# Optimization experiments

Hardware: AMD Instinct MI355X
Metric: run time of the kernel (lower is better)

The kernel has to match this reference:

```python
import jax, jax.numpy as jnp
import numpy as np

B, S, HID, NH = 4, 2048, 512, 8
DH = HID // NH
NEG = -1000000.0


def setup_inputs() -> dict:
    key = jax.random.key(0)
    ks = jax.random.split(key, 8)
    scale = 1.0 / np.sqrt(HID)
    return {
        "queries": jax.random.normal(ks[0], (B, S, HID), dtype=jnp.float32),
        "keys": jax.random.normal(ks[1], (B, S, HID), dtype=jnp.float32),
        "values": jax.random.normal(ks[2], (B, S, HID), dtype=jnp.float32),
        "valid_lens": jax.random.randint(ks[3], (B,), 1, S + 1, dtype=jnp.int32),
        "Wq": jax.random.uniform(ks[4], (HID, HID), jnp.float32, -scale, scale),
        "Wk": jax.random.uniform(ks[5], (HID, HID), jnp.float32, -scale, scale),
        "Wv": jax.random.uniform(ks[6], (HID, HID), jnp.float32, -scale, scale),
        "Wo": jax.random.uniform(ks[7], (HID, HID), jnp.float32, -scale, scale),
    }


def _split_heads(x):
    # (B, S, HID) -> (B, NH, S, DH)
    return x.reshape(B, S, NH, DH).transpose(0, 2, 1, 3)


def reference(queries, keys, values, valid_lens, Wq, Wk, Wv, Wo):
    q = _split_heads(queries @ Wq.T)
    k = _split_heads(keys @ Wk.T)
    v = _split_heads(values @ Wv.T)
    scores = jnp.einsum("bhqd,bhkd->bhqk", q, k) / jnp.sqrt(jnp.float32(DH))
    # valid_lens is per-batch; mask key positions >= valid_len with -1e6 (as in sequence_mask)
    mask = jnp.arange(S)[None, :] < valid_lens[:, None]          # (B, S)
    scores = jnp.where(mask[:, None, None, :], scores, NEG)
    attn = jax.nn.softmax(scores, axis=-1)
    out = jnp.einsum("bhqk,bhkd->bhqd", attn, v)                 # (B, NH, S, DH)
    out = out.transpose(0, 2, 1, 3).reshape(B, S, HID)
    return out @ Wo.T
```

## Files before the change

kernel.cpp:

```cpp
#include <hip/hip_runtime.h>

#define B_ 4
#define S_ 2048
#define HIDN 512
#define NH 8
#define DH 64

typedef __attribute__((ext_vector_type(8))) short short8;
typedef __attribute__((ext_vector_type(4))) short short4v;
typedef __attribute__((ext_vector_type(8))) __bf16 bf16x8;
typedef __attribute__((ext_vector_type(4))) float floatx4;
typedef __attribute__((ext_vector_type(2))) unsigned uint2v;
typedef __attribute__((ext_vector_type(4))) unsigned uint4v;

__device__ inline short f2bf(float f) {
    union { float f; unsigned u; } x; x.f = f;
    unsigned r = x.u + 0x7fffu + ((x.u >> 16) & 1u);
    return (short)(r >> 16);
}

__device__ inline unsigned pack2(float a, float b) {
    unsigned ua = __builtin_bit_cast(unsigned, a) + 0x8000u;
    unsigned ub = __builtin_bit_cast(unsigned, b) + 0x8000u;
    return __builtin_amdgcn_perm(ub, ua, 0x07060302);
}

__device__ inline short8 cvt8(const float* __restrict__ p) {
    floatx4 f0 = *(const floatx4*)p;
    floatx4 f1 = *(const floatx4*)(p + 4);
    uint4v u;
    u[0] = pack2(f0[0], f0[1]); u[1] = pack2(f0[2], f0[3]);
    u[2] = pack2(f1[0], f1[1]); u[3] = pack2(f1[2], f1[3]);
    return __builtin_bit_cast(short8, u);
}

__device__ inline floatx4 mfma_s(short8 a, short8 b, floatx4 c) {
    return __builtin_amdgcn_mfma_f32_16x16x32_bf16(
        __builtin_bit_cast(bf16x8, a), __builtin_bit_cast(bf16x8, b), c, 0, 0, 0);
}

__device__ inline float vmax4(floatx4 v) {
    return fmaxf(fmaxf(v[0], v[1]), fmaxf(v[2], v[3]));
}

__global__ void cvt_w(const float* __restrict__ wq, const float* __restrict__ wk,
                      const float* __restrict__ wv, short* __restrict__ out) {
    const float* src = blockIdx.y == 0 ? wq : (blockIdx.y == 1 ? wk : wv);
    int i = (blockIdx.x * 256 + threadIdx.x) * 4;
    floatx4 f = *(const floatx4*)&src[i];
    short4v v; v[0]=f2bf(f[0]); v[1]=f2bf(f[1]); v[2]=f2bf(f[2]); v[3]=f2bf(f[3]);
    *(short4v*)&out[blockIdx.y * (HIDN * HIDN) + i] = v;
}

__global__ __launch_bounds__(256) void gemm_qkv(const float* __restrict__ xq,
                                                const float* __restrict__ xk,
                                                const float* __restrict__ xv,
                                                const short* __restrict__ wb,
                                                short* __restrict__ Qh,
                                                short* __restrict__ Kh,
                                                short* __restrict__ VT) {
    const int z = blockIdx.z;
    const float* X = z == 0 ? xq : (z == 1 ? xk : xv);
    const short* W = wb + z * (HIDN * HIDN);
    short* dstQK = z == 0 ? Qh : Kh;

    __shared__ __align__(16) short Als[128][72];
    __shared__ __align__(16) short Bls[128][72];

    const int t = threadIdx.x;
    const int w = t >> 6, lane = t & 63, quad = lane >> 4, l16 = lane & 15;
    const int wm = (w & 1) * 64, wn = (w >> 1) * 64;
    const int m0 = blockIdx.x * 128, n0 = blockIdx.y * 128;

    floatx4 acc[4][4];
    floatx4 zero = {0.f, 0.f, 0.f, 0.f};
#pragma unroll
    for (int i = 0; i < 4; i++)
#pragma unroll
        for (int j = 0; j < 4; j++) acc[i][j] = zero;

    const int row0 = t >> 3;
    const int c8 = (t & 7) * 8;

    for (int k0 = 0; k0 < HIDN; k0 += 64) {
        __syncthreads();
#pragma unroll
        for (int rr = 0; rr < 4; rr++)
            *(short8*)&Als[row0 + rr*32][c8] =
                cvt8(&X[(m0 + row0 + rr*32) * HIDN + k0 + c8]);
#pragma unroll
        for (int rr = 0; rr < 4; rr++)
            *(short8*)&Bls[row0 + rr*32][c8] =
                *(const short8*)&W[(n0 + row0 + rr*32) * HIDN + k0 + c8];
        __syncthreads();

#pragma unroll
        for (int ks = 0; ks < 2; ks++) {
            const int cq8 = (ks * 4 + quad) * 8;
            short8 a[4], b[4];
#pragma unroll
            for (int i = 0; i < 4; i++)
                a[i] = *(const short8*)&Als[wm + i*16 + l16][cq8];
#pragma unroll
            for (int j = 0; j < 4; j++)
                b[j] = *(const short8*)&Bls[wn + j*16 + l16][cq8];
#pragma unroll
            for (int i = 0; i < 4; i++)
#pragma unroll
                for (int j = 0; j < 4; j++)
                    acc[i][j] = mfma_s(a[i], b[j], acc[i][j]);
        }
    }

    if (z < 2) {
#pragma unroll
        for (int i = 0; i < 4; i++)
#pragma unroll
            for (int j = 0; j < 4; j++)
#pragma unroll
                for (int r = 0; r < 4; r++) {
                    int m = m0 + wm + i*16 + quad*4 + r;
                    int n = n0 + wn + j*16 + l16;
                    int bb = m >> 11, s = m & 2047, h = n >> 6, d = n & 63;
                    dstQK[((bb * NH + h) * S_ + s) * DH + d] = f2bf(acc[i][j][r]);
                }
    } else {
#pragma unroll
        for (int i = 0; i < 4; i++)
#pragma unroll
            for (int j = 0; j < 4; j++) {
                int s0 = m0 + wm + i*16 + quad*4;
                int n = n0 + wn + j*16 + l16;
                int bb = s0 >> 11, s = s0 & 2047, h = n >> 6, d = n & 63;
                uint2v v;
                v[0] = pack2(acc[i][j][0], acc[i][j][1]);
                v[1] = pack2(acc[i][j][2], acc[i][j][3]);
                *(uint2v*)&VT[((bb * NH + h) * DH + d) * S_ + s] = v;
            }
    }
}

__global__ __launch_bounds__(256) void gemm_out(const short* __restrict__ AO,
                                                const float* __restrict__ Wo,
                                                float* __restrict__ C) {
    __shared__ __align__(16) short Als[128][72];
    __shared__ __align__(16) short Bls[64][72];

    const int t = threadIdx.x;
    const int w = t >> 6, lane = t & 63, quad = lane >> 4, l16 = lane & 15;
    const int wm = (w & 1) * 64, wn = (w >> 1) * 32;
    const int m0 = blockIdx.x * 128, n0 = blockIdx.y * 64;

    floatx4 acc[4][2];
    floatx4 zero = {0.f, 0.f, 0.f, 0.f};
#pragma unroll
    for (int i = 0; i < 4; i++)
#pragma unroll
        for (int j = 0; j < 2; j++) acc[i][j] = zero;

    const int row0 = t >> 3;
    const int c8 = (t & 7) * 8;

    for (int k0 = 0; k0 < HIDN; k0 += 64) {
        __syncthreads();
#pragma unroll
        for (int rr = 0; rr < 4; rr++)
            *(short8*)&Als[row0 + rr*32][c8] =
                *(const short8*)&AO[(m0 + row0 + rr*32) * HIDN + k0 + c8];
#pragma unroll
        for (int rr = 0; rr < 2; rr++)
            *(short8*)&Bls[row0 + rr*32][c8] =
                cvt8(&Wo[(n0 + row0 + rr*32) * HIDN + k0 + c8]);
        __syncthreads();

#pragma unroll
        for (int ks = 0; ks < 2; ks++) {
            const int cq8 = (ks * 4 + quad) * 8;
            short8 a[4], b[2];
#pragma unroll
            for (int i = 0; i < 4; i++)
                a[i] = *(const short8*)&Als[wm + i*16 + l16][cq8];
#pragma unroll
            for (int j = 0; j < 2; j++)
                b[j] = *(const short8*)&Bls[wn + j*16 + l16][cq8];
#pragma unroll
            for (int i = 0; i < 4; i++)
#pragma unroll
                for (int j = 0; j < 2; j++)
                    acc[i][j] = mfma_s(a[i], b[j], acc[i][j]);
        }
    }

#pragma unroll
    for (int i = 0; i < 4; i++)
#pragma unroll
        for (int j = 0; j < 2; j++)
#pragma unroll
            for (int r = 0; r < 4; r++) {
                int m = m0 + wm + i*16 + quad*4 + r;
                int n = n0 + wn + j*16 + l16;
                C[m * HIDN + n] = acc[i][j][r];
            }
}

__global__ __launch_bounds__(256, 4) void attn_kernel(const short* __restrict__ Qh,
                                                      const short* __restrict__ Kh,
                                                      const short* __restrict__ VT,
                                                      const int* __restrict__ vlen,
                                                      short* __restrict__ AO) {
    __shared__ __align__(16) short Ksh[128 * 64];
    __shared__ __align__(16) short Vsh[64 * 128];
    short* Psh = Ksh;

    const int t = threadIdx.x, w = t >> 6, lane = t & 63;
    const int quad = lane >> 4, l16 = lane & 15;
    const int qb = blockIdx.x * 64;
    const int h = blockIdx.y, b = blockIdx.z;
    const int bh = b * NH + h;
    const int vl = vlen[b];
    const int nfull = vl >> 7, rem = vl & 127;
    const int nt = nfull + (rem ? 1 : 0);

    const float SC = 0.180336879f;

    const short* qrow = &Qh[(bh * S_ + qb + w * 16 + l16) * DH];
    short8 qa0 = *(const short8*)&qrow[quad * 8];
    short8 qa1 = *(const short8*)&qrow[32 + quad * 8];

    float m_run = -1e30f, l_run = 0.f;
    floatx4 Oacc[4];
    floatx4 zero = {0.f, 0.f, 0.f, 0.f};
#pragma unroll
    for (int dt = 0; dt < 4; dt++) Oacc[dt] = zero;

    for (int kt = 0; kt < nt; kt++) {
        const int base = kt << 7;
        const bool bnd = (base + 128) > vl;
        __syncthreads();
        {
            const short* Kg = &Kh[(bh * S_ + base) * DH];
#pragma unroll
            for (int it = 0; it < 4; it++) {
                int idx = it * 256 + t;
                int row = idx >> 3, c = idx & 7;
                *(short8*)&Ksh[row * 64 + (((c ^ (row & 7))) << 3)] =
                    *(const short8*)&Kg[row * DH + (c << 3)];
            }
            const short* Vg = &VT[bh * DH * S_ + base];
#pragma unroll
            for (int it = 0; it < 4; it++) {
                int idx = it * 256 + t;
                int d = idx >> 4, c = idx & 15;
                *(short8*)&Vsh[d * 128 + (((c ^ (d & 7))) << 3)] =
                    *(const short8*)&Vg[d * S_ + (c << 3)];
            }
        }
        __syncthreads();

        floatx4 sc[8];
#pragma unroll
        for (int n = 0; n < 8; n++) {
            int krow = n * 16 + l16;
            const short* kr = &Ksh[krow * 64];
            short8 kb0 = *(const short8*)&kr[((quad ^ (krow & 7)) << 3)];
            short8 kb1 = *(const short8*)&kr[(((4 + quad) ^ (krow & 7)) << 3)];
            floatx4 s = zero;
            s = mfma_s(kb0, qa0, s);
            s = mfma_s(kb1, qa1, s);
            sc[n] = s;
        }
        __syncthreads();

        if (!bnd) {
#pragma unroll
            for (int n = 0; n < 8; n++)
#pragma unroll
                for (int r = 0; r < 4; r++) sc[n][r] *= SC;
        } else {
#pragma unroll
            for (int n = 0; n < 8; n++)
#pragma unroll
                for (int r = 0; r < 4; r++) {
                    int key = base + n * 16 + quad * 4 + r;
                    sc[n][r] = (key < vl) ? sc[n][r] * SC : -1e30f;
                }
        }

        float mx = vmax4(sc[0]);
#pragma unroll
        for (int n = 1; n < 8; n++) mx = fmaxf(mx, vmax4(sc[n]));
        mx = fmaxf(mx, __shfl_xor(mx, 16));
        mx = fmaxf(mx, __shfl_xor(mx, 32));
        float mnew = fmaxf(m_run, mx);
        float alpha = __builtin_amdgcn_exp2f(m_run - mnew);
        m_run = mnew;
        float rs = 0.f;
#pragma unroll
        for (int n = 0; n < 8; n++)
#pragma unroll
            for (int r = 0; r < 4; r++) {
                float p = __builtin_amdgcn_exp2f(sc[n][r] - mnew);
                sc[n][r] = p;
                rs += p;
            }
        rs += __shfl_xor(rs, 16);
        rs += __shfl_xor(rs, 32);
        l_run = l_run * alpha + rs;
#pragma unroll
        for (int dt = 0; dt < 4; dt++)
#pragma unroll
            for (int r = 0; r < 4; r++) Oacc[dt][r] *= alpha;

#pragma unroll
        for (int n = 0; n < 8; n++) {
            unsigned lo = pack2(sc[n][0], sc[n][1]);
            unsigned hi = pack2(sc[n][2], sc[n][3]);
            int c = (n << 1) + (quad >> 1);
            int idx = (w << 11) + (l16 << 7) + ((c ^ (l16 & 7)) << 3) + ((quad & 1) << 2);
            uint2v pv; pv[0] = lo; pv[1] = hi;
            *(uint2v*)&Psh[idx] = pv;
        }
        __syncthreads();

#pragma unroll
        for (int kk = 0; kk < 4; kk++) {
            int pc = (kk << 2) + quad;
            short8 pf = *(const short8*)&Psh[(w << 11) + (l16 << 7) + ((pc ^ (l16 & 7)) << 3)];
#pragma unroll
            for (int dt = 0; dt < 4; dt++) {
                int vrow = dt * 16 + l16;
                short8 vf = *(const short8*)&Vsh[vrow * 128 + ((pc ^ (vrow & 7)) << 3)];
                Oacc[dt] = mfma_s(vf, pf, Oacc[dt]);
            }
        }
    }

    float inv = 1.0f / l_run;
    int q = qb + w * 16 + l16;
    short* dst = &AO[(b * S_ + q) * HIDN + h * DH];
#pragma unroll
    for (int dt = 0; dt < 4; dt++) {
        uint2v v;
        v[0] = pack2(Oacc[dt][0] * inv, Oacc[dt][1] * inv);
        v[1] = pack2(Oacc[dt][2] * inv, Oacc[dt][3] * inv);
        *(uint2v*)&dst[dt * 16 + quad * 4] = v;
    }
}

extern "C" void kernel_launch(void* const* d_in, const int* in_sizes, int n_in,
                              void* d_out, int out_size, void* d_ws, size_t ws_size,
                              hipStream_t stream) {
    const float* q  = (const float*)d_in[0];
    const float* k  = (const float*)d_in[1];
    const float* v  = (const float*)d_in[2];
    const int*   vl = (const int*)d_in[3];
    const float* wq = (const float*)d_in[4];
    const float* wk = (const float*)d_in[5];
    const float* wv = (const float*)d_in[6];
    const float* wo = (const float*)d_in[7];
    float* out = (float*)d_out;

    const size_t HSZ = (size_t)B_ * NH * S_ * DH;
    short* Qh  = (short*)d_ws;
    short* Kh  = Qh + HSZ;
    short* VT  = Kh + HSZ;
    short* AO  = VT + HSZ;
    short* Wqkv = AO;

    dim3 blk(256);
    cvt_w<<<dim3(256, 3), blk, 0, stream>>>(wq, wk, wv, Wqkv);
    gemm_qkv<<<dim3(64, 4, 3), blk, 0, stream>>>(q, k, v, Wqkv, Qh, Kh, VT);
    attn_kernel<<<dim3(S_ / 64, NH, B_), blk, 0, stream>>>(Qh, Kh, VT, vl, AO);
    gemm_out<<<dim3(64, 8), blk, 0, stream>>>(AO, wo, out);
}
```

Baseline: 174.0 us.

## Prefetch next K/V tile into registers, fold scale into exp, skip rescale

Loads the next K and V tiles from global memory into registers while the current tile is being computed, with the shared-memory addresses computed once up front. The softmax scale is now folded into the exp argument through an fma, and the output-accumulator rescale is skipped when no lane's running max changes. The barrier between the P writes and P reads becomes a wait on the local data share only, which is valid because each wave reads only its own P slice. This adds register pressure from the prefetch buffers, which could reduce occupancy under the launch bounds of 256 threads and 4 blocks.

```diff
diff --git a/kernel.cpp b/kernel.cpp
--- a/kernel.cpp
+++ b/kernel.cpp
@@ -218,8 +218,7 @@
     const int h = blockIdx.y, b = blockIdx.z;
     const int bh = b * NH + h;
     const int vl = vlen[b];
-    const int nfull = vl >> 7, rem = vl & 127;
-    const int nt = nfull + (rem ? 1 : 0);
+    const int nt = (vl + 127) >> 7;
 
     const float SC = 0.180336879f;
 
@@ -227,6 +226,30 @@
     short8 qa0 = *(const short8*)&qrow[quad * 8];
     short8 qa1 = *(const short8*)&qrow[32 + quad * 8];
 
+    const int krow = t >> 3;
+    const int kc = t & 7;
+    const int vd = t >> 4;
+    const int vc = t & 15;
+    int kgo[4], klo[4], vgo[4], vlo[4];
+#pragma unroll
+    for (int it = 0; it < 4; it++) {
+        const int kr_ = krow + it * 32;
+        kgo[it] = kr_ * DH + (kc << 3);
+        klo[it] = kr_ * 64 + ((kc ^ (kr_ & 7)) << 3);
+        const int vd_ = vd + it * 16;
+        vgo[it] = vd_ * S_ + (vc << 3);
+        vlo[it] = vd_ * 128 + ((vc ^ (vd_ & 7)) << 3);
+    }
+
+    const short* Kgb = &Kh[(size_t)bh * S_ * DH];
+    const short* Vgb = &VT[(size_t)bh * DH * S_];
+
+    short8 krg[4], vrg[4];
+#pragma unroll
+    for (int it = 0; it < 4; it++) krg[it] = *(const short8*)&Kgb[kgo[it]];
+#pragma unroll
+    for (int it = 0; it < 4; it++) vrg[it] = *(const short8*)&Vgb[vgo[it]];
+
     float m_run = -1e30f, l_run = 0.f;
     floatx4 Oacc[4];
     floatx4 zero = {0.f, 0.f, 0.f, 0.f};
@@ -236,34 +259,31 @@
     for (int kt = 0; kt < nt; kt++) {
         const int base = kt << 7;
         const bool bnd = (base + 128) > vl;
-        __syncthreads();
-        {
-            const short* Kg = &Kh[(bh * S_ + base) * DH];
-#pragma unroll
-            for (int it = 0; it < 4; it++) {
-                int idx = it * 256 + t;
-                int row = idx >> 3, c = idx & 7;
-                *(short8*)&Ksh[row * 64 + (((c ^ (row & 7))) << 3)] =
-                    *(const short8*)&Kg[row * DH + (c << 3)];
-            }
-            const short* Vg = &VT[bh * DH * S_ + base];
-#pragma unroll
-            for (int it = 0; it < 4; it++) {
-                int idx = it * 256 + t;
-                int d = idx >> 4, c = idx & 15;
-                *(short8*)&Vsh[d * 128 + (((c ^ (d & 7))) << 3)] =
-                    *(const short8*)&Vg[d * S_ + (c << 3)];
-            }
-        }
-        __syncthreads();
+
+        __syncthreads();
+#pragma unroll
+        for (int it = 0; it < 4; it++) *(short8*)&Ksh[klo[it]] = krg[it];
+#pragma unroll
+        for (int it = 0; it < 4; it++) *(short8*)&Vsh[vlo[it]] = vrg[it];
+        __syncthreads();
+
+        if (kt + 1 < nt) {
+            const int nb = (kt + 1) << 7;
+#pragma unroll
+            for (int it = 0; it < 4; it++)
+                krg[it] = *(const short8*)&Kgb[nb * DH + kgo[it]];
+#pragma unroll
+            for (int it = 0; it < 4; it++)
+                vrg[it] = *(const short8*)&Vgb[nb + vgo[it]];
+        }
 
         floatx4 sc[8];
 #pragma unroll
         for (int n = 0; n < 8; n++) {
-            int krow = n * 16 + l16;
-            const short* kr = &Ksh[krow * 64];
-            short8 kb0 = *(const short8*)&kr[((quad ^ (krow & 7)) << 3)];
-            short8 kb1 = *(const short8*)&kr[(((4 + quad) ^ (krow & 7)) << 3)];
+            int kro = n * 16 + l16;
+            const short* kr = &Ksh[kro * 64];
+            short8 kb0 = *(const short8*)&kr[((quad ^ (kro & 7)) << 3)];
+            short8 kb1 = *(const short8*)&kr[(((4 + quad) ^ (kro & 7)) << 3)];
             floatx4 s = zero;
             s = mfma_s(kb0, qa0, s);
             s = mfma_s(kb1, qa1, s);
@@ -271,18 +291,13 @@
         }
         __syncthreads();
 
-        if (!bnd) {
-#pragma unroll
-            for (int n = 0; n < 8; n++)
-#pragma unroll
-                for (int r = 0; r < 4; r++) sc[n][r] *= SC;
-        } else {
+        if (bnd) {
 #pragma unroll
             for (int n = 0; n < 8; n++)
 #pragma unroll
                 for (int r = 0; r < 4; r++) {
                     int key = base + n * 16 + quad * 4 + r;
-                    sc[n][r] = (key < vl) ? sc[n][r] * SC : -1e30f;
+                    if (key >= vl) sc[n][r] = -1e30f;
                 }
         }
 
@@ -291,25 +306,29 @@
         for (int n = 1; n < 8; n++) mx = fmaxf(mx, vmax4(sc[n]));
         mx = fmaxf(mx, __shfl_xor(mx, 16));
         mx = fmaxf(mx, __shfl_xor(mx, 32));
-        float mnew = fmaxf(m_run, mx);
-        float alpha = __builtin_amdgcn_exp2f(m_run - mnew);
+        const float mxs = mx * SC;
+        const bool norescale = __all(mxs <= m_run);
+        const float mnew = norescale ? m_run : fmaxf(m_run, mxs);
+        const float alpha = norescale ? 1.0f : __builtin_amdgcn_exp2f(m_run - mnew);
         m_run = mnew;
         float rs = 0.f;
 #pragma unroll
         for (int n = 0; n < 8; n++)
 #pragma unroll
             for (int r = 0; r < 4; r++) {
-                float p = __builtin_amdgcn_exp2f(sc[n][r] - mnew);
+                float p = __builtin_amdgcn_exp2f(fmaf(sc[n][r], SC, -mnew));
                 sc[n][r] = p;
                 rs += p;
             }
         rs += __shfl_xor(rs, 16);
         rs += __shfl_xor(rs, 32);
         l_run = l_run * alpha + rs;
-#pragma unroll
-        for (int dt = 0; dt < 4; dt++)
-#pragma unroll
-            for (int r = 0; r < 4; r++) Oacc[dt][r] *= alpha;
+        if (!norescale) {
+#pragma unroll
+            for (int dt = 0; dt < 4; dt++)
+#pragma unroll
+                for (int r = 0; r < 4; r++) Oacc[dt][r] *= alpha;
+        }
 
 #pragma unroll
         for (int n = 0; n < 8; n++) {
@@ -320,7 +339,8 @@
             uint2v pv; pv[0] = lo; pv[1] = hi;
             *(uint2v*)&Psh[idx] = pv;
         }
-        __syncthreads();
+        asm volatile("s_waitcnt lgkmcnt(0)" ::: "memory");
+        __builtin_amdgcn_sched_barrier(0);
 
 #pragma unroll
         for (int kk = 0; kk < 4; kk++) {
```

Result: slower. 184.5 us (+6.0%).

## Pre-convert inputs to bf16 and use direct global-to-LDS loads in projection GEMMs

Applied to the files above, without the earlier changes.

Adds separate conversion kernels that turn the fp32 activations and all four weight matrices into bf16 workspace buffers. New QKV and output-projection GEMMs then stream the bf16 tiles straight into LDS with global_load_lds, using 128x128 tiles. The goal is to take fp32 loading and conversion out of the GEMM inner loops and simplify their memory traffic. In exchange it adds an extra full read and write of the activations and a larger workspace requirement, with the old path kept as a fallback when the workspace is too small.

```diff
diff --git a/kernel.cpp b/kernel.cpp
--- a/kernel.cpp
+++ b/kernel.cpp
@@ -43,8 +43,181 @@
     return fmaxf(fmaxf(v[0], v[1]), fmaxf(v[2], v[3]));
 }
 
-__global__ void cvt_w(const float* __restrict__ wq, const float* __restrict__ wk,
-                      const float* __restrict__ wv, short* __restrict__ out) {
+__device__ inline void gl_lds(const short* g, short* l) {
+    __builtin_amdgcn_global_load_lds(
+        (const __attribute__((address_space(1))) void*)g,
+        (__attribute__((address_space(3))) void*)l, 16, 0, 0);
+}
+
+__global__ void cvt_x(const float* __restrict__ xq, const float* __restrict__ xk,
+                      const float* __restrict__ xv, short* __restrict__ out) {
+    const float* src = blockIdx.y == 0 ? xq : (blockIdx.y == 1 ? xk : xv);
+    int i = (blockIdx.x * 256 + threadIdx.x) * 8;
+    *(short8*)&out[(size_t)blockIdx.y * (B_ * S_ * HIDN) + i] = cvt8(&src[i]);
+}
+
+__global__ void cvt_w4(const float* __restrict__ wq, const float* __restrict__ wk,
+                       const float* __restrict__ wv, const float* __restrict__ wo,
+                       short* __restrict__ out) {
+    const float* src = blockIdx.y == 0 ? wq :
+                       (blockIdx.y == 1 ? wk : (blockIdx.y == 2 ? wv : wo));
+    int i = (blockIdx.x * 256 + threadIdx.x) * 8;
+    *(short8*)&out[blockIdx.y * (HIDN * HIDN) + i] = cvt8(&src[i]);
+}
+
+__global__ __launch_bounds__(256) void gemm_qkv2(const short* __restrict__ Xb,
+                                                 const short* __restrict__ wb,
+                                                 short* __restrict__ Qh,
+                                                 short* __restrict__ Kh,
+                                                 short* __restrict__ VT) {
+    const int z = blockIdx.z;
+    const short* X = Xb + (size_t)z * (B_ * S_ * HIDN);
+    const short* W = wb + z * (HIDN * HIDN);
+    short* dstQK = z == 0 ? Qh : Kh;
+
+    __shared__ __align__(16) short Als[128 * 64];
+    __shared__ __align__(16) short Bls[128 * 64];
+
+    const int t = threadIdx.x;
+    const int w = t >> 6, lane = t & 63, quad = lane >> 4, l16 = lane & 15;
+    const int wm = (w & 1) * 64, wn = (w >> 1) * 64;
+    const int m0 = blockIdx.x * 128, n0 = blockIdx.y * 128;
+
+    floatx4 acc[4][4];
+    floatx4 zero = {0.f, 0.f, 0.f, 0.f};
+#pragma unroll
+    for (int i = 0; i < 4; i++)
+#pragma unroll
+        for (int j = 0; j < 4; j++) acc[i][j] = zero;
+
+    const int srow = t >> 3;
+    const int sc8 = (t & 7) * 8;
+    const int ldsb = (t & ~63) * 8;
+
+    for (int k0 = 0; k0 < HIDN; k0 += 64) {
+        __syncthreads();
+#pragma unroll
+        for (int it = 0; it < 4; it++)
+            gl_lds(&X[(size_t)(m0 + srow + it * 32) * HIDN + k0 + sc8],
+                   &Als[it * 2048 + ldsb]);
+#pragma unroll
+        for (int it = 0; it < 4; it++)
+            gl_lds(&W[(n0 + srow + it * 32) * HIDN + k0 + sc8],
+                   &Bls[it * 2048 + ldsb]);
+        __syncthreads();
+
+#pragma unroll
+        for (int ks = 0; ks < 2; ks++) {
+            const int cq8 = (ks * 4 + quad) * 8;
+            short8 a[4], b[4];
+#pragma unroll
+            for (int i = 0; i < 4; i++)
+                a[i] = *(const short8*)&Als[(wm + i * 16 + l16) * 64 + cq8];
+#pragma unroll
+            for (int j = 0; j < 4; j++)
+                b[j] = *(const short8*)&Bls[(wn + j * 16 + l16) * 64 + cq8];
+#pragma unroll
+            for (int i = 0; i < 4; i++)
+#pragma unroll
+                for (int j = 0; j < 4; j++)
+                    acc[i][j] = mfma_s(a[i], b[j], acc[i][j]);
+        }
+    }
+
+    if (z < 2) {
+#pragma unroll
+        for (int i = 0; i < 4; i++)
+#pragma unroll
+            for (int j = 0; j < 4; j++)
+#pragma unroll
+                for (int r = 0; r < 4; r++) {
+                    int m = m0 + wm + i*16 + quad*4 + r;
+                    int n = n0 + wn + j*16 + l16;
+                    int bb = m >> 11, s = m & 2047, h = n >> 6, d = n & 63;
+                    dstQK[((bb * NH + h) * S_ + s) * DH + d] = f2bf(acc[i][j][r]);
+                }
+    } else {
+#pragma unroll
+        for (int i = 0; i < 4; i++)
+#pragma unroll
+            for (int j = 0; j < 4; j++) {
+                int s0 = m0 + wm + i*16 + quad*4;
+                int n = n0 + wn + j*16 + l16;
+                int bb = s0 >> 11, s = s0 & 2047, h = n >> 6, d = n & 63;
+                uint2v v;
+                v[0] = pack2(acc[i][j][0], acc[i][j][1]);
+                v[1] = pack2(acc[i][j][2], acc[i][j][3]);
+                *(uint2v*)&VT[((bb * NH + h) * DH + d) * S_ + s] = v;
+            }
+    }
+}
+
+__global__ __launch_bounds__(256) void gemm_out2(const short* __restrict__ AO,
+                                                 const short* __restrict__ WoB,
+                                                 float* __restrict__ C) {
+    __shared__ __align__(16) short Als[128 * 64];
+    __shared__ __align__(16) short Bls[128 * 64];
+
+    const int t = threadIdx.x;
+    const int w = t >> 6, lane = t & 63, quad = lane >> 4, l16 = lane & 15;
+    const int wm = (w & 1) * 64, wn = (w >> 1) * 64;
+    const int m0 = blockIdx.x * 128, n0 = blockIdx.y * 128;
+
+    floatx4 acc[4][4];
+    floatx4 zero = {0.f, 0.f, 0.f, 0.f};
+#pragma unroll
+    for (int i = 0; i < 4; i++)
+#pragma unroll
+        for (int j = 0; j < 4; j++) acc[i][j] = zero;
+
+    const int srow = t >> 3;
+    const int sc8 = (t & 7) * 8;
+    const int ldsb = (t & ~63) * 8;
+
+    for (int k0 = 0; k0 < HIDN; k0 += 64) {
+        __syncthreads();
+#pragma unroll
+        for (int it = 0; it < 4; it++)
+            gl_lds(&AO[(size_t)(m0 + srow + it * 32) * HIDN + k0 + sc8],
+                   &Als[it * 2048 + ldsb]);
+#pragma unroll
+        for (int it = 0; it < 4; it++)
+            gl_lds(&WoB[(n0 + srow + it * 32) * HIDN + k0 + sc8],
+                   &Bls[it * 2048 + ldsb]);
+        __syncthreads();
+
+#pragma unroll
+        for (int ks = 0; ks < 2; ks++) {
+            const int cq8 = (ks * 4 + quad) * 8;
+            short8 a[4], b[4];
+#pragma unroll
+            for (int i = 0; i < 4; i++)
+                a[i] = *(const short8*)&Als[(wm + i * 16 + l16) * 64 + cq8];
+#pragma unroll
+            for (int j = 0; j < 4; j++)
+                b[j] = *(const short8*)&Bls[(wn + j * 16 + l16) * 64 + cq8];
+#pragma unroll
+            for (int i = 0; i < 4; i++)
+#pragma unroll
+                for (int j = 0; j < 4; j++)
+                    acc[i][j] = mfma_s(a[i], b[j], acc[i][j]);
+        }
+    }
+
+#pragma unroll
+    for (int i = 0; i < 4; i++)
+#pragma unroll
+        for (int j = 0; j < 4; j++)
+#pragma unroll
+            for (int r = 0; r < 4; r++) {
+                int m = m0 + wm + i*16 + quad*4 + r;
+                int n = n0 + wn + j*16 + l16;
+                C[m * HIDN + n] = acc[i][j][r];
+            }
+}
+
+__global__ void cvt_w3(const float* __restrict__ wq, const float* __restrict__ wk,
+                       const float* __restrict__ wv, short* __restrict__ out) {
     const float* src = blockIdx.y == 0 ? wq : (blockIdx.y == 1 ? wk : wv);
     int i = (blockIdx.x * 256 + threadIdx.x) * 4;
     floatx4 f = *(const floatx4*)&src[i];
@@ -361,15 +534,29 @@
     float* out = (float*)d_out;
 
     const size_t HSZ = (size_t)B_ * NH * S_ * DH;
+    const size_t WSZ = (size_t)HIDN * HIDN;
+
     short* Qh  = (short*)d_ws;
     short* Kh  = Qh + HSZ;
     short* VT  = Kh + HSZ;
     short* AO  = VT + HSZ;
-    short* Wqkv = AO;
 
     dim3 blk(256);
-    cvt_w<<<dim3(256, 3), blk, 0, stream>>>(wq, wk, wv, Wqkv);
-    gemm_qkv<<<dim3(64, 4, 3), blk, 0, stream>>>(q, k, v, Wqkv, Qh, Kh, VT);
-    attn_kernel<<<dim3(S_ / 64, NH, B_), blk, 0, stream>>>(Qh, Kh, VT, vl, AO);
-    gemm_out<<<dim3(64, 8), blk, 0, stream>>>(AO, wo, out);
-}
+    const size_t need = (4 * HSZ + 3 * HSZ + 4 * WSZ) * sizeof(short);
+
+    if (ws_size >= need) {
+        short* Xb = AO + HSZ;
+        short* Wb = Xb + 3 * HSZ;
+        cvt_x<<<dim3(2048, 3), blk, 0, stream>>>(q, k, v, Xb);
+        cvt_w4<<<dim3(128, 4), blk, 0, stream>>>(wq, wk, wv, wo, Wb);
+        gemm_qkv2<<<dim3(64, 4, 3), blk, 0, stream>>>(Xb, Wb, Qh, Kh, VT);
+        attn_kernel<<<dim3(S_ / 64, NH, B_), blk, 0, stream>>>(Qh, Kh, VT, vl, AO);
+        gemm_out2<<<dim3(64, 4), blk, 0, stream>>>(AO, Wb + 3 * WSZ, out);
+    } else {
+        short* Wqkv = AO;
+        cvt_w3<<<dim3(256, 3), blk, 0, stream>>>(wq, wk, wv, Wqkv);
+        gemm_qkv<<<dim3(64, 4, 3), blk, 0, stream>>>(q, k, v, Wqkv, Qh, Kh, VT);
+        attn_kernel<<<dim3(S_ / 64, NH, B_), blk, 0, stream>>>(Qh, Kh, VT, vl, AO);
+        gemm_out<<<dim3(64, 8), blk, 0, stream>>>(AO, wo, out);
+    }
+}
```

After: 186.6 us. +7.3%, slower.
